# Kernel optimization log

Hardware: AMD Instinct MI355X
Metric: run time of the kernel (lower is better)

The kernel has to match this reference:

```python
import jax, jax.numpy as jnp
import numpy as np

HIDDEN = 4096
NUM_Q = 32
NUM_KV = 8
HEAD_DIM = 128
EPS = 1e-6
ROPE_THETA = 1e6


def _rmsnorm(x, w):
    # x: [..., HEAD_DIM]
    var = jnp.mean(x * x, axis=-1, keepdims=True)
    return x * jax.lax.rsqrt(var + EPS) * w


def _rope(x, positions):
    # x: [n_tok, H, HEAD_DIM], rotate-half convention
    half = HEAD_DIM // 2
    inv_freq = 1.0 / (ROPE_THETA ** (jnp.arange(0, half, dtype=jnp.float32) / half))
    freqs = positions.astype(jnp.float32)[:, None] * inv_freq  # [n_tok, half]
    cos = jnp.concatenate([jnp.cos(freqs), jnp.cos(freqs)], axis=-1)[:, None, :]
    sin = jnp.concatenate([jnp.sin(freqs), jnp.sin(freqs)], axis=-1)[:, None, :]
    x1, x2 = x[..., :half], x[..., half:]
    rot = jnp.concatenate([-x2, x1], axis=-1)
    return x * cos + rot * sin


def setup_inputs() -> dict:
    key = jax.random.key(0)
    ks = jax.random.split(key, 7)
    n_tok = 2048
    s = 0.02
    return {
        "hidden": jax.random.normal(ks[0], (n_tok, HIDDEN), dtype=jnp.float32),
        "positions": jnp.arange(n_tok, dtype=jnp.int32),
        "Wq": jax.random.normal(ks[1], (HIDDEN, NUM_Q * HEAD_DIM), dtype=jnp.float32) * s,
        "Wk": jax.random.normal(ks[2], (HIDDEN, NUM_KV * HEAD_DIM), dtype=jnp.float32) * s,
        "Wv": jax.random.normal(ks[3], (HIDDEN, NUM_KV * HEAD_DIM), dtype=jnp.float32) * s,
        "Wo": jax.random.normal(ks[4], (NUM_Q * HEAD_DIM, HIDDEN), dtype=jnp.float32) * s,
        "q_norm_w": jnp.ones((HEAD_DIM,), dtype=jnp.float32),
        "k_norm_w": jnp.ones((HEAD_DIM,), dtype=jnp.float32),
    }


def reference(hidden, positions, Wq, Wk, Wv, Wo, q_norm_w, k_norm_w):
    n_tok = hidden.shape[0]
    group = NUM_Q // NUM_KV

    q = (hidden @ Wq).reshape(n_tok, NUM_Q, HEAD_DIM)
    k = (hidden @ Wk).reshape(n_tok, NUM_KV, HEAD_DIM)
    v = (hidden @ Wv).reshape(n_tok, NUM_KV, HEAD_DIM)

    q = _rmsnorm(q, q_norm_w)
    k = _rmsnorm(k, k_norm_w)
    q = _rope(q, positions)
    k = _rope(k, positions)

    # GQA: group q heads [n_tok, NUM_KV, group, HEAD_DIM]
    qg = q.reshape(n_tok, NUM_KV, group, HEAD_DIM)
    scale = 1.0 / np.sqrt(HEAD_DIM)
    scores = jnp.einsum("qhgd,khd->hgqk", qg, k) * scale  # [NUM_KV, group, n_tok, n_tok]
    causal = jnp.tril(jnp.ones((n_tok, n_tok), dtype=bool))
    scores = jnp.where(causal, scores, jnp.finfo(scores.dtype).min)
    probs = jax.nn.softmax(scores, axis=-1)
    out = jnp.einsum("hgqk,khd->qhgd", probs, v)  # [n_tok, NUM_KV, group, HEAD_DIM]
    out = out.reshape(n_tok, NUM_Q * HEAD_DIM)
    return out @ Wo
```

## Files before the change

### kernel.cpp

```cpp
#include <hip/hip_runtime.h>
#include <stdint.h>

typedef unsigned short u16;
typedef __bf16 bf16_t;
typedef bf16_t bf16x8 __attribute__((ext_vector_type(8)));
typedef float f32x4 __attribute__((ext_vector_type(4)));
typedef u16 u16x4 __attribute__((ext_vector_type(4)));
typedef u16 u16x8 __attribute__((ext_vector_type(8)));

#define HIDDEN 4096
#define NTOK 2048
#define NQ 32
#define NKV 8
#define HD 128
#define QKV_N 6144

#define AS1 __attribute__((address_space(1)))
#define AS3 __attribute__((address_space(3)))

__device__ __forceinline__ u16 f2bf(float f) {
  union { float f; uint32_t u; } v; v.f = f;
  uint32_t u = v.u;
  return (u16)((u + 0x7fffu + ((u >> 16) & 1u)) >> 16);
}

__global__ void cvt_hidden(const float* __restrict__ src, u16* __restrict__ dst, int n4) {
  int i = blockIdx.x * blockDim.x + threadIdx.x;
  if (i >= n4) return;
  float4 v = ((const float4*)src)[i];
  u16x4 o;
  o[0] = f2bf(v.x); o[1] = f2bf(v.y); o[2] = f2bf(v.z); o[3] = f2bf(v.w);
  ((u16x4*)dst)[i] = o;
}

__global__ void transpose_cvt(const float* __restrict__ src, u16* __restrict__ dst,
                              int R, int C) {
  __shared__ float tile[64][65];
  int tx = threadIdx.x & 63;
  int ty = threadIdx.x >> 6;
  int r0 = blockIdx.y * 64, c0 = blockIdx.x * 64;
  for (int i = 0; i < 16; i++) {
    int r = ty + i * 4;
    tile[r][tx] = src[(size_t)(r0 + r) * C + c0 + tx];
  }
  __syncthreads();
  for (int i = 0; i < 16; i++) {
    int c = ty + i * 4;
    dst[(size_t)(c0 + c) * R + r0 + tx] = f2bf(tile[tx][c]);
  }
}

__global__ __launch_bounds__(256, 3) void gemm_bt(const u16* __restrict__ A,
                                                  const u16* __restrict__ B,
                                                  float* __restrict__ C,
                                                  int M, int N, int K) {
  __shared__ u16 sA[128 * 64];
  __shared__ u16 sB[128 * 64];
  const int tid = threadIdx.x;
  const int wave = tid >> 6, lane = tid & 63;
  const int quad = lane >> 4, l16 = lane & 15;
  const int wy = wave >> 1, wx = wave & 1;
  const int row0 = blockIdx.y * 128, col0 = blockIdx.x * 128;
  f32x4 acc[4][4] = {};
  const int lr = lane >> 3;
  const int sc = (lane & 7) ^ lr;
  const u16* gA = A + (size_t)(row0 + wave * 32 + lr) * K + sc * 8;
  const u16* gB = B + (size_t)(col0 + wave * 32 + lr) * K + sc * 8;
  u16* lA = sA + wave * 32 * 64;
  u16* lB = sB + wave * 32 * 64;
  const int swz = l16 & 7;
  for (int k0 = 0; k0 < K; k0 += 64) {
    for (int j = 0; j < 4; j++) {
      __builtin_amdgcn_global_load_lds(
          (AS1 void*)(void*)(gA + k0 + (size_t)(j * 8) * K),
          (AS3 void*)(void*)(lA + j * 8 * 64), 16, 0, 0);
      __builtin_amdgcn_global_load_lds(
          (AS1 void*)(void*)(gB + k0 + (size_t)(j * 8) * K),
          (AS3 void*)(void*)(lB + j * 8 * 64), 16, 0, 0);
    }
    __syncthreads();
    bf16x8 af[2][4], bfr[2][4];
    for (int s = 0; s < 2; s++)
      for (int mi = 0; mi < 4; mi++) {
        const int c = ((s * 4 + quad) ^ swz) * 8;
        af[s][mi] = *(const bf16x8*)(const void*)(sA + (wy * 64 + mi * 16 + l16) * 64 + c);
        bfr[s][mi] = *(const bf16x8*)(const void*)(sB + (wx * 64 + mi * 16 + l16) * 64 + c);
      }
    for (int s = 0; s < 2; s++)
      for (int mi = 0; mi < 4; mi++)
        for (int ni = 0; ni < 4; ni++)
          acc[mi][ni] = __builtin_amdgcn_mfma_f32_16x16x32_bf16(af[s][mi], bfr[s][ni], acc[mi][ni], 0, 0, 0);
    __syncthreads();
  }
  for (int mi = 0; mi < 4; mi++)
    for (int ni = 0; ni < 4; ni++) {
      int row = row0 + wy * 64 + mi * 16 + quad * 4;
      int col = col0 + wx * 64 + ni * 16 + l16;
      float* cp = C + (size_t)row * N + col;
      for (int r = 0; r < 4; r++) cp[(size_t)r * N] = acc[mi][ni][r];
    }
}

__global__ void normrope(const float* __restrict__ qkv, const int* __restrict__ pos,
                         const float* __restrict__ qw, const float* __restrict__ kw,
                         u16* __restrict__ Qo, u16* __restrict__ Ko) {
  const int hh = blockIdx.x;
  const int t = blockIdx.y * 4 + (threadIdx.x >> 6);
  const int lane = threadIdx.x & 63;
  const bool isQ = hh < NQ;
  const int col = isQ ? hh * HD : HIDDEN + (hh - NQ) * HD;
  const float* src = qkv + (size_t)t * QKV_N + col;
  float x1 = src[lane], x2 = src[lane + 64];
  float ss = x1 * x1 + x2 * x2;
  for (int m = 1; m < 64; m <<= 1) ss += __shfl_xor(ss, m);
  float inv = rsqrtf(ss * (1.0f / 128.0f) + 1e-6f);
  const float* w = isQ ? qw : kw;
  x1 *= inv * w[lane];
  x2 *= inv * w[lane + 64];
  float p = (float)pos[t];
  float freq = expf((float)lane * -0.2158673525f);
  float a = p * freq;
  float sn = sinf(a), cs = cosf(a);
  float o1 = x1 * cs - x2 * sn;
  float o2 = x2 * cs + x1 * sn;
  const float osc = isQ ? 0.08838834764831845f : 1.0f;
  u16* dst = isQ ? (Qo + (size_t)t * (NQ * HD) + hh * HD)
                 : (Ko + (size_t)t * (NKV * HD) + (hh - NQ) * HD);
  dst[lane] = f2bf(o1 * osc);
  dst[lane + 64] = f2bf(o2 * osc);
}

__global__ void vtrans(const float* __restrict__ qkv, u16* __restrict__ vT) {
  __shared__ float s[128][65];
  int tb = blockIdx.x;
  int vh = blockIdx.y;
  int tid = threadIdx.x;
  for (int i = 0; i < 32; i++) {
    int e = i * 256 + tid;
    int tl = e >> 7;
    int d = e & 127;
    s[d][tl] = qkv[(size_t)(tb * 64 + tl) * QKV_N + 5120 + vh * 128 + d];
  }
  __syncthreads();
  for (int i = 0; i < 32; i++) {
    int e = i * 256 + tid;
    int d = e >> 6;
    int tl = e & 63;
    vT[(size_t)vh * (HD * NTOK) + (size_t)d * NTOK + tb * 64 + tl] = f2bf(s[d][tl]);
  }
}

__global__ __launch_bounds__(512) void flash2(const u16* __restrict__ Q,
                                              const u16* __restrict__ K,
                                              const u16* __restrict__ V,
                                              u16* __restrict__ O) {
  __shared__ u16 sK[64 * 136];
  __shared__ u16 sV[128 * 72];
  __shared__ u16 sP[8][16 * 72];
  const int p = blockIdx.x, h = blockIdx.y, kvh = h >> 2;
  const int tid = threadIdx.x;
  const int wave = tid >> 6, lane = tid & 63;
  const int quad = lane >> 4, l16 = lane & 15;
  u16* myP = &sP[wave][0];
  const u16* Vh = V + (size_t)kvh * (HD * NTOK);
  const int qtiles[2] = {p, 15 - p};
  const int rk0 = tid >> 4, ck0 = tid & 15;
  const int rv0 = tid >> 3, cv0 = tid & 7;
  for (int ti = 0; ti < 2; ti++) {
    const int qb = qtiles[ti];
    const int qrow0 = qb * 128 + wave * 16;
    bf16x8 qf[4];
    for (int ks = 0; ks < 4; ks++)
      qf[ks] = *(const bf16x8*)(const void*)(Q + (size_t)(qrow0 + l16) * (NQ * HD) + h * HD + ks * 32 + quad * 8);
    f32x4 accO[8] = {};
    float l_r[4] = {0.f, 0.f, 0.f, 0.f};
    const int nU = 2 * (qb + 1);
    const int myMax = (qrow0 + 15) >> 6;
    for (int kb = 0; kb < nU; kb++) {
      u16x8 k0 = *(const u16x8*)(const void*)(K + (size_t)(kb * 64 + rk0) * (NKV * HD) + kvh * HD + ck0 * 8);
      u16x8 k1 = *(const u16x8*)(const void*)(K + (size_t)(kb * 64 + rk0 + 32) * (NKV * HD) + kvh * HD + ck0 * 8);
      u16x8 v0 = *(const u16x8*)(const void*)(Vh + (size_t)rv0 * NTOK + kb * 64 + cv0 * 8);
      u16x8 v1 = *(const u16x8*)(const void*)(Vh + (size_t)(rv0 + 64) * NTOK + kb * 64 + cv0 * 8);
      __syncthreads();
      *(u16x8*)(void*)(sK + rk0 * 136 + ck0 * 8) = k0;
      *(u16x8*)(void*)(sK + (rk0 + 32) * 136 + ck0 * 8) = k1;
      *(u16x8*)(void*)(sV + rv0 * 72 + cv0 * 8) = v0;
      *(u16x8*)(void*)(sV + (rv0 + 64) * 72 + cv0 * 8) = v1;
      __syncthreads();
      if (kb <= myMax) {
        f32x4 s[4] = {};
        for (int ks = 0; ks < 4; ks++)
          for (int nt = 0; nt < 4; nt++) {
            bf16x8 kf = *(const bf16x8*)(const void*)(sK + (nt * 16 + l16) * 136 + ks * 32 + quad * 8);
            s[nt] = __builtin_amdgcn_mfma_f32_16x16x32_bf16(qf[ks], kf, s[nt], 0, 0, 0);
          }
        const int qg = qrow0 + quad * 4;
        for (int nt = 0; nt < 4; nt++) {
          int tok = kb * 64 + nt * 16 + l16;
          for (int r = 0; r < 4; r++) {
            float e = __expf(s[nt][r]);
            float pv = (tok <= qg + r) ? e : 0.0f;
            l_r[r] += pv;
            myP[(quad * 4 + r) * 72 + nt * 16 + l16] = f2bf(pv);
          }
        }
        asm volatile("s_waitcnt lgkmcnt(0)" ::: "memory");
        for (int ks = 0; ks < 2; ks++) {
          bf16x8 pf = *(const bf16x8*)(const void*)(myP + l16 * 72 + ks * 32 + quad * 8);
          for (int nt = 0; nt < 8; nt++) {
            bf16x8 vf = *(const bf16x8*)(const void*)(sV + (nt * 16 + l16) * 72 + ks * 32 + quad * 8);
            accO[nt] = __builtin_amdgcn_mfma_f32_16x16x32_bf16(pf, vf, accO[nt], 0, 0, 0);
          }
        }
      }
    }
    float inv[4];
    for (int r = 0; r < 4; r++) {
      float t = l_r[r];
      t += __shfl_xor(t, 1);
      t += __shfl_xor(t, 2);
      t += __shfl_xor(t, 4);
      t += __shfl_xor(t, 8);
      inv[r] = 1.0f / t;
    }
    for (int nt = 0; nt < 8; nt++)
      for (int r = 0; r < 4; r++)
        O[(size_t)(qrow0 + quad * 4 + r) * (NQ * HD) + h * HD + nt * 16 + l16] =
            f2bf(accO[nt][r] * inv[r]);
  }
}

extern "C" void kernel_launch(void* const* d_in, const int* in_sizes, int n_in,
                              void* d_out, int out_size, void* d_ws, size_t ws_size,
                              hipStream_t stream) {
  const float* hidden = (const float*)d_in[0];
  const int* positions = (const int*)d_in[1];
  const float* Wq = (const float*)d_in[2];
  const float* Wk = (const float*)d_in[3];
  const float* Wv = (const float*)d_in[4];
  const float* Wo = (const float*)d_in[5];
  const float* qw = (const float*)d_in[6];
  const float* kw = (const float*)d_in[7];
  char* ws = (char*)d_ws;
  u16* hid_bf  = (u16*)(ws);
  u16* WqkvT   = (u16*)(ws + 16777216);
  u16* WoT     = (u16*)(ws + 67108864);
  float* qkvf  = (float*)(ws + 100663296);
  u16* Qn      = (u16*)(ws + 150994944);
  u16* Kn      = (u16*)(ws + 167772160);
  u16* Vt      = (u16*)(ws + 171966464);
  u16* AO      = (u16*)(ws + 176160768);
  float* outp  = (float*)d_out;

  cvt_hidden<<<NTOK * HIDDEN / 4 / 256, 256, 0, stream>>>(hidden, hid_bf, NTOK * HIDDEN / 4);
  transpose_cvt<<<dim3(64, 64), 256, 0, stream>>>(Wq, WqkvT, 4096, 4096);
  transpose_cvt<<<dim3(16, 64), 256, 0, stream>>>(Wk, WqkvT + (size_t)4096 * 4096, 4096, 1024);
  transpose_cvt<<<dim3(16, 64), 256, 0, stream>>>(Wv, WqkvT + (size_t)5120 * 4096, 4096, 1024);
  transpose_cvt<<<dim3(64, 64), 256, 0, stream>>>(Wo, WoT, 4096, 4096);
  gemm_bt<<<dim3(48, 16), 256, 0, stream>>>(hid_bf, WqkvT, qkvf, 2048, 6144, 4096);
  normrope<<<dim3(40, 512), 256, 0, stream>>>(qkvf, positions, qw, kw, Qn, Kn);
  vtrans<<<dim3(32, 8), 256, 0, stream>>>(qkvf, Vt);
  flash2<<<dim3(8, 32), 512, 0, stream>>>(Qn, Kn, Vt, AO);
  gemm_bt<<<dim3(32, 16), 256, 0, stream>>>(AO, WoT, outp, 2048, 4096, 4096);
}
```

Measured before the change: 502.3 us.

## Fuse QKV GEMM with RMSNorm, RoPE and V transpose; merge prep kernels

The QKV GEMM epilogue now performs per-head RMSNorm, RoPE, scaling and bf16 conversion directly from accumulators, and writes V transposed. This removes the fp32 qkv intermediate and the separate normrope and vtrans kernels. The hidden conversion and the four weight transposes are merged into one launch that uses vectorized float4 loads and 8-wide stores. Each block's N-tile is remapped so one head's two halves pair up for RoPE, which makes the epilogue heavier with cross-wave shared-memory reductions and sin/cos work per element.

New measurement: 1.367 ms. 172% more time.

```diff
diff --git a/kernel.cpp b/kernel.cpp
--- a/kernel.cpp
+++ b/kernel.cpp
@@ -24,30 +24,156 @@
   return (u16)((u + 0x7fffu + ((u >> 16) & 1u)) >> 16);
 }
 
-__global__ void cvt_hidden(const float* __restrict__ src, u16* __restrict__ dst, int n4) {
-  int i = blockIdx.x * blockDim.x + threadIdx.x;
-  if (i >= n4) return;
-  float4 v = ((const float4*)src)[i];
-  u16x4 o;
-  o[0] = f2bf(v.x); o[1] = f2bf(v.y); o[2] = f2bf(v.z); o[3] = f2bf(v.w);
-  ((u16x4*)dst)[i] = o;
-}
-
-__global__ void transpose_cvt(const float* __restrict__ src, u16* __restrict__ dst,
-                              int R, int C) {
+__global__ __launch_bounds__(256) void prep(
+    const float* __restrict__ hidden, u16* __restrict__ hid_bf,
+    const float* __restrict__ Wq, const float* __restrict__ Wk,
+    const float* __restrict__ Wv, const float* __restrict__ Wo,
+    u16* __restrict__ WqkvT, u16* __restrict__ WoT) {
   __shared__ float tile[64][65];
-  int tx = threadIdx.x & 63;
-  int ty = threadIdx.x >> 6;
-  int r0 = blockIdx.y * 64, c0 = blockIdx.x * 64;
-  for (int i = 0; i < 16; i++) {
-    int r = ty + i * 4;
-    tile[r][tx] = src[(size_t)(r0 + r) * C + c0 + tx];
+  int b = blockIdx.x;
+  int t = threadIdx.x;
+  if (b < 8192) {
+    int i = b * 256 + t;
+    float4 v = ((const float4*)hidden)[i];
+    u16x4 o; o[0]=f2bf(v.x); o[1]=f2bf(v.y); o[2]=f2bf(v.z); o[3]=f2bf(v.w);
+    ((u16x4*)hid_bf)[i] = o;
+    return;
+  }
+  b -= 8192;
+  const float* src; u16* dst; int C;
+  if (b < 4096)      { src = Wq; dst = WqkvT;                     C = 4096; }
+  else if (b < 5120) { src = Wk; dst = WqkvT + (size_t)4096*4096; C = 1024; b -= 4096; }
+  else if (b < 6144) { src = Wv; dst = WqkvT + (size_t)5120*4096; C = 1024; b -= 5120; }
+  else               { src = Wo; dst = WoT;                       C = 4096; b -= 6144; }
+  const int R = 4096;
+  int ntx = C >> 6;
+  int r0 = (b / ntx) * 64, c0 = (b % ntx) * 64;
+  int lr = t >> 4, lc = (t & 15) * 4;
+  for (int i = 0; i < 4; i++) {
+    float4 v = *(const float4*)&src[(size_t)(r0 + lr + i * 16) * C + c0 + lc];
+    tile[lr + i * 16][lc + 0] = v.x;
+    tile[lr + i * 16][lc + 1] = v.y;
+    tile[lr + i * 16][lc + 2] = v.z;
+    tile[lr + i * 16][lc + 3] = v.w;
   }
   __syncthreads();
-  for (int i = 0; i < 16; i++) {
-    int c = ty + i * 4;
-    dst[(size_t)(c0 + c) * R + r0 + tx] = f2bf(tile[tx][c]);
-  }
+  int oc = t >> 3, orr = (t & 7) * 8;
+  for (int i = 0; i < 2; i++) {
+    int c = oc + i * 32;
+    u16x8 o;
+    for (int e = 0; e < 8; e++) o[e] = f2bf(tile[orr + e][c]);
+    *(u16x8*)&dst[(size_t)(c0 + c) * R + r0 + orr] = o;
+  }
+}
+
+__global__ __launch_bounds__(256, 3) void gemm_qkv(
+    const u16* __restrict__ A, const u16* __restrict__ B,
+    const int* __restrict__ pos,
+    const float* __restrict__ qw, const float* __restrict__ kw,
+    u16* __restrict__ Qn, u16* __restrict__ Kn, u16* __restrict__ Vt) {
+  const int K = 4096;
+  __shared__ u16 sA[128 * 64];
+  __shared__ u16 sB[128 * 64];
+  __shared__ float S[2][2][4][16];
+  const int tid = threadIdx.x;
+  const int wave = tid >> 6, lane = tid & 63;
+  const int quad = lane >> 4, l16 = lane & 15;
+  const int wy = wave >> 1, wx = wave & 1;
+  const int h = blockIdx.x;
+  const int row0 = blockIdx.y * 128;
+  f32x4 acc[4][4] = {};
+  const int lr = lane >> 3;
+  const int sc = (lane & 7) ^ lr;
+  const u16* gA = A + (size_t)(row0 + wave * 32 + lr) * K + sc * 8;
+  const u16* gB = B + (size_t)(h * 128 + wave * 32 + lr) * K + sc * 8;
+  u16* lA = sA + wave * 32 * 64;
+  u16* lB = sB + wave * 32 * 64;
+  const int swz = l16 & 7;
+  for (int k0 = 0; k0 < K; k0 += 64) {
+    for (int j = 0; j < 4; j++) {
+      __builtin_amdgcn_global_load_lds(
+          (AS1 void*)(void*)(gA + k0 + (size_t)(j * 8) * K),
+          (AS3 void*)(void*)(lA + j * 8 * 64), 16, 0, 0);
+      __builtin_amdgcn_global_load_lds(
+          (AS1 void*)(void*)(gB + k0 + (size_t)(j * 8) * K),
+          (AS3 void*)(void*)(lB + j * 8 * 64), 16, 0, 0);
+    }
+    __syncthreads();
+    bf16x8 af[2][4], bfr[2][4];
+    for (int s = 0; s < 2; s++) {
+      const int c = ((s * 4 + quad) ^ swz) * 8;
+      for (int mi = 0; mi < 4; mi++)
+        af[s][mi] = *(const bf16x8*)(const void*)(sA + (wy * 64 + mi * 16 + l16) * 64 + c);
+      for (int ni = 0; ni < 4; ni++)
+        bfr[s][ni] = *(const bf16x8*)(const void*)(sB + (wx * 16 + ni * 32 + l16) * 64 + c);
+    }
+    for (int s = 0; s < 2; s++)
+      for (int mi = 0; mi < 4; mi++)
+        for (int ni = 0; ni < 4; ni++)
+          acc[mi][ni] = __builtin_amdgcn_mfma_f32_16x16x32_bf16(af[s][mi], bfr[s][ni], acc[mi][ni], 0, 0, 0);
+    __syncthreads();
+  }
+  if (h >= 40) {
+    int vh = h - 40;
+    for (int mi = 0; mi < 4; mi++) {
+      int t0 = row0 + wy * 64 + mi * 16 + quad * 4;
+      for (int ni = 0; ni < 4; ni++) {
+        int d = wx * 16 + ni * 32 + l16;
+        u16x4 o;
+        for (int r = 0; r < 4; r++) o[r] = f2bf(acc[mi][ni][r]);
+        *(u16x4*)&Vt[(size_t)vh * (HD * NTOK) + (size_t)d * NTOK + t0] = o;
+      }
+    }
+    return;
+  }
+  f32x4 ssv[4];
+  for (int mi = 0; mi < 4; mi++)
+    for (int r = 0; r < 4; r++) {
+      float s = 0.f;
+      for (int ni = 0; ni < 4; ni++) s += acc[mi][ni][r] * acc[mi][ni][r];
+      ssv[mi][r] = s;
+    }
+  for (int m = 1; m < 16; m <<= 1)
+    for (int mi = 0; mi < 4; mi++)
+      for (int r = 0; r < 4; r++)
+        ssv[mi][r] += __shfl_xor(ssv[mi][r], m);
+  S[wx][wy][quad][l16] = ssv[l16 >> 2][l16 & 3];
+  __syncthreads();
+  f32x4 invv[4];
+  for (int mi = 0; mi < 4; mi++) {
+    f32x4 oss = *(const f32x4*)&S[1 - wx][wy][quad][mi * 4];
+    for (int r = 0; r < 4; r++)
+      invv[mi][r] = rsqrtf((ssv[mi][r] + oss[r]) * (1.0f / 128.0f) + 1e-6f);
+  }
+  const bool isQ = (h < 32);
+  const float* w = isQ ? qw : kw;
+  const float osc = isQ ? 0.08838834764831845f : 1.0f;
+  float w1[2], w2[2], fr[2];
+  for (int ni = 0; ni < 2; ni++) {
+    int d = wx * 16 + ni * 32 + l16;
+    w1[ni] = w[d];
+    w2[ni] = w[d + 64];
+    fr[ni] = exp2f(-0.3114307588956805f * (float)d);
+  }
+  u16* dstb; int ld;
+  if (isQ) { dstb = Qn + h * 128; ld = NQ * HD; }
+  else     { dstb = Kn + (h - 32) * 128; ld = NKV * HD; }
+  for (int mi = 0; mi < 4; mi++)
+    for (int r = 0; r < 4; r++) {
+      int t = row0 + wy * 64 + mi * 16 + quad * 4 + r;
+      float p = (float)pos[t];
+      float s_ = invv[mi][r] * osc;
+      u16* rowp = dstb + (size_t)t * ld;
+      for (int ni = 0; ni < 2; ni++) {
+        int d = wx * 16 + ni * 32 + l16;
+        float a1 = acc[mi][ni][r] * w1[ni];
+        float a2 = acc[mi][ni + 2][r] * w2[ni];
+        float ang = p * fr[ni];
+        float sn = sinf(ang), cs = cosf(ang);
+        rowp[d]      = f2bf((a1 * cs - a2 * sn) * s_);
+        rowp[d + 64] = f2bf((a2 * cs + a1 * sn) * s_);
+      }
+    }
 }
 
 __global__ __launch_bounds__(256, 3) void gemm_bt(const u16* __restrict__ A,
@@ -80,12 +206,13 @@
     }
     __syncthreads();
     bf16x8 af[2][4], bfr[2][4];
-    for (int s = 0; s < 2; s++)
+    for (int s = 0; s < 2; s++) {
+      const int c = ((s * 4 + quad) ^ swz) * 8;
       for (int mi = 0; mi < 4; mi++) {
-        const int c = ((s * 4 + quad) ^ swz) * 8;
         af[s][mi] = *(const bf16x8*)(const void*)(sA + (wy * 64 + mi * 16 + l16) * 64 + c);
         bfr[s][mi] = *(const bf16x8*)(const void*)(sB + (wx * 64 + mi * 16 + l16) * 64 + c);
       }
+    }
     for (int s = 0; s < 2; s++)
       for (int mi = 0; mi < 4; mi++)
         for (int ni = 0; ni < 4; ni++)
@@ -99,55 +226,6 @@
       float* cp = C + (size_t)row * N + col;
       for (int r = 0; r < 4; r++) cp[(size_t)r * N] = acc[mi][ni][r];
     }
-}
-
-__global__ void normrope(const float* __restrict__ qkv, const int* __restrict__ pos,
-                         const float* __restrict__ qw, const float* __restrict__ kw,
-                         u16* __restrict__ Qo, u16* __restrict__ Ko) {
-  const int hh = blockIdx.x;
-  const int t = blockIdx.y * 4 + (threadIdx.x >> 6);
-  const int lane = threadIdx.x & 63;
-  const bool isQ = hh < NQ;
-  const int col = isQ ? hh * HD : HIDDEN + (hh - NQ) * HD;
-  const float* src = qkv + (size_t)t * QKV_N + col;
-  float x1 = src[lane], x2 = src[lane + 64];
-  float ss = x1 * x1 + x2 * x2;
-  for (int m = 1; m < 64; m <<= 1) ss += __shfl_xor(ss, m);
-  float inv = rsqrtf(ss * (1.0f / 128.0f) + 1e-6f);
-  const float* w = isQ ? qw : kw;
-  x1 *= inv * w[lane];
-  x2 *= inv * w[lane + 64];
-  float p = (float)pos[t];
-  float freq = expf((float)lane * -0.2158673525f);
-  float a = p * freq;
-  float sn = sinf(a), cs = cosf(a);
-  float o1 = x1 * cs - x2 * sn;
-  float o2 = x2 * cs + x1 * sn;
-  const float osc = isQ ? 0.08838834764831845f : 1.0f;
-  u16* dst = isQ ? (Qo + (size_t)t * (NQ * HD) + hh * HD)
-                 : (Ko + (size_t)t * (NKV * HD) + (hh - NQ) * HD);
-  dst[lane] = f2bf(o1 * osc);
-  dst[lane + 64] = f2bf(o2 * osc);
-}
-
-__global__ void vtrans(const float* __restrict__ qkv, u16* __restrict__ vT) {
-  __shared__ float s[128][65];
-  int tb = blockIdx.x;
-  int vh = blockIdx.y;
-  int tid = threadIdx.x;
-  for (int i = 0; i < 32; i++) {
-    int e = i * 256 + tid;
-    int tl = e >> 7;
-    int d = e & 127;
-    s[d][tl] = qkv[(size_t)(tb * 64 + tl) * QKV_N + 5120 + vh * 128 + d];
-  }
-  __syncthreads();
-  for (int i = 0; i < 32; i++) {
-    int e = i * 256 + tid;
-    int d = e >> 6;
-    int tl = e & 63;
-    vT[(size_t)vh * (HD * NTOK) + (size_t)d * NTOK + tb * 64 + tl] = f2bf(s[d][tl]);
-  }
 }
 
 __global__ __launch_bounds__(512) void flash2(const u16* __restrict__ Q,
@@ -243,23 +321,16 @@
   const float* kw = (const float*)d_in[7];
   char* ws = (char*)d_ws;
   u16* hid_bf  = (u16*)(ws);
-  u16* WqkvT   = (u16*)(ws + 16777216);
-  u16* WoT     = (u16*)(ws + 67108864);
-  float* qkvf  = (float*)(ws + 100663296);
-  u16* Qn      = (u16*)(ws + 150994944);
-  u16* Kn      = (u16*)(ws + 167772160);
-  u16* Vt      = (u16*)(ws + 171966464);
-  u16* AO      = (u16*)(ws + 176160768);
+  u16* WqkvT   = (u16*)(ws + (size_t)16*1048576);
+  u16* WoT     = (u16*)(ws + (size_t)64*1048576);
+  u16* Qn      = (u16*)(ws + (size_t)96*1048576);
+  u16* Kn      = (u16*)(ws + (size_t)112*1048576);
+  u16* Vt      = (u16*)(ws + (size_t)116*1048576);
+  u16* AO      = (u16*)(ws + (size_t)120*1048576);
   float* outp  = (float*)d_out;
 
-  cvt_hidden<<<NTOK * HIDDEN / 4 / 256, 256, 0, stream>>>(hidden, hid_bf, NTOK * HIDDEN / 4);
-  transpose_cvt<<<dim3(64, 64), 256, 0, stream>>>(Wq, WqkvT, 4096, 4096);
-  transpose_cvt<<<dim3(16, 64), 256, 0, stream>>>(Wk, WqkvT + (size_t)4096 * 4096, 4096, 1024);
-  transpose_cvt<<<dim3(16, 64), 256, 0, stream>>>(Wv, WqkvT + (size_t)5120 * 4096, 4096, 1024);
-  transpose_cvt<<<dim3(64, 64), 256, 0, stream>>>(Wo, WoT, 4096, 4096);
-  gemm_bt<<<dim3(48, 16), 256, 0, stream>>>(hid_bf, WqkvT, qkvf, 2048, 6144, 4096);
-  normrope<<<dim3(40, 512), 256, 0, stream>>>(qkvf, positions, qw, kw, Qn, Kn);
-  vtrans<<<dim3(32, 8), 256, 0, stream>>>(qkvf, Vt);
+  prep<<<18432, 256, 0, stream>>>(hidden, hid_bf, Wq, Wk, Wv, Wo, WqkvT, WoT);
+  gemm_qkv<<<dim3(48, 16), 256, 0, stream>>>(hid_bf, WqkvT, positions, qw, kw, Qn, Kn, Vt);
   flash2<<<dim3(8, 32), 512, 0, stream>>>(Qn, Kn, Vt, AO);
   gemm_bt<<<dim3(32, 16), 256, 0, stream>>>(AO, WoT, outp, 2048, 4096, 4096);
 }
```
